# Kernel optimization log

Measured on AMD Instinct MI355X. Metric: run time of the kernel, lower is better.

Reference implementation:

```python
import jax, jax.numpy as jnp
import numpy as np

VOCAB, DIM, LAYERS, HEADS, FF, SEQ, BATCH = 32000, 1024, 4, 16, 4096, 2048, 2
HD = DIM // HEADS
EPS = 1e-6
ROPE_BASE = 10000.0


def setup_inputs() -> dict:
    key = jax.random.key(0)
    ks = jax.random.split(key, 10)
    std = 0.02
    return {
        "input_ids": jax.random.randint(ks[0], (BATCH, SEQ), 0, VOCAB, dtype=jnp.int32),
        "emb": jax.random.normal(ks[1], (VOCAB, DIM), jnp.float32) * std,
        "qkv_w": jax.random.normal(ks[2], (LAYERS, 3 * DIM, DIM), jnp.float32) * std,
        "out_w": jax.random.normal(ks[3], (LAYERS, DIM, DIM), jnp.float32) * std,
        "fc1_w": jax.random.normal(ks[4], (LAYERS, FF, DIM), jnp.float32) * std,
        "fc2_w": jax.random.normal(ks[5], (LAYERS, DIM, FF), jnp.float32) * std,
        "norm1_s": jnp.ones((LAYERS, DIM), jnp.float32),
        "norm2_s": jnp.ones((LAYERS, DIM), jnp.float32),
        "normf_s": jnp.ones((DIM,), jnp.float32),
        "lm_w": jax.random.normal(ks[6], (VOCAB, DIM), jnp.float32) * std,
    }


def _rms(x, scale):
    return x * jax.lax.rsqrt(jnp.mean(x * x, axis=-1, keepdims=True) + EPS) * scale


def _rope_tables(seq_len):
    inv_freq = 1.0 / (ROPE_BASE ** (jnp.arange(0, HD, 2, dtype=jnp.float32) / HD))
    freqs = jnp.arange(seq_len, dtype=jnp.float32)[:, None] * inv_freq[None, :]  # [S, HD/2]
    emb = jnp.concatenate([freqs, freqs], axis=-1)  # [S, HD]
    return jnp.cos(emb), jnp.sin(emb)


def _rotate_half(x):
    x1, x2 = jnp.split(x, 2, axis=-1)
    return jnp.concatenate([-x2, x1], axis=-1)


def _attention(h, qkv_w, out_w, cos, sin, mask):
    B, S, _ = h.shape
    qkv = jnp.einsum('bsd,ed->bse', h, qkv_w)  # [B, S, 3*DIM]
    qkv = qkv.reshape(B, S, 3, HEADS, HD).transpose(2, 0, 3, 1, 4)  # [3, B, H, S, hd]
    q, k, v = qkv[0], qkv[1], qkv[2]
    q = q * cos + _rotate_half(q) * sin
    k = k * cos + _rotate_half(k) * sin
    scores = jnp.einsum('bhqd,bhkd->bhqk', q, k) * (HD ** -0.5)
    scores = jnp.where(mask, scores, -jnp.inf)
    attn = jax.nn.softmax(scores, axis=-1)
    out = jnp.einsum('bhqk,bhkd->bhqd', attn, v)
    out = out.transpose(0, 2, 1, 3).reshape(B, S, DIM)
    return jnp.einsum('bsd,ed->bse', out, out_w)


def reference(input_ids, emb, qkv_w, out_w, fc1_w, fc2_w, norm1_s, norm2_s, normf_s, lm_w):
    B, S = input_ids.shape
    x = emb[input_ids]  # [B, S, DIM]
    cos, sin = _rope_tables(S)
    mask = jnp.tril(jnp.ones((S, S), dtype=bool))  # causal
    for l in range(LAYERS):
        x = x + _attention(_rms(x, norm1_s[l]), qkv_w[l], out_w[l], cos, sin, mask)
        h = _rms(x, norm2_s[l])
        ff = jnp.einsum('bsf,df->bsd', jax.nn.silu(jnp.einsum('bsd,fd->bsf', h, fc1_w[l])), fc2_w[l])
        x = x + ff
    logits = jnp.einsum('bsd,vd->bsv', _rms(x, normf_s), lm_w)
    return logits
```

## Files before the change

kernel.cpp:

```cpp
#include <hip/hip_runtime.h>

using u16 = unsigned short;
using u32 = unsigned int;
using bf16x8 = __attribute__((ext_vector_type(8))) __bf16;
using u16x8  = __attribute__((ext_vector_type(8))) u16;
using f32x4  = __attribute__((ext_vector_type(4))) float;
using u32x4  = __attribute__((ext_vector_type(4))) u32;

#define SEQ    2048
#define BATCH  2
#define DIM    1024
#define HEADS  16
#define HD     64
#define FF     4096
#define LAYERS 4
#define VOCAB  32000
#define ROWS   (BATCH*SEQ)

__device__ __forceinline__ u16 f2bf(float f) {
  u32 u = __float_as_uint(f);
  u += 0x7fffu + ((u >> 16) & 1u);
  return (u16)(u >> 16);
}
__device__ __forceinline__ float bf2f(u16 h) { return __uint_as_float(((u32)h) << 16); }

__device__ __forceinline__ void gload_lds16(const u16* g, u16* l) {
  __builtin_amdgcn_global_load_lds(
      (__attribute__((address_space(1))) void*)(u16*)g,
      (__attribute__((address_space(3))) void*)l, 16, 0, 0);
}

constexpr int BM = 128, BN = 128, BK = 32;

template<int EPI>
__global__ __launch_bounds__(256)
void gemm_nt(const u16* __restrict__ A, const u16* __restrict__ Bw,
             float* __restrict__ Cf, u16* __restrict__ Cb,
             int M, int N, int K, int KH)
{
  __shared__ __align__(16) u16 As[2][BM*BK];
  __shared__ __align__(16) u16 Bs[2][BN*BK];
  const int tid  = threadIdx.x;
  const int wid  = tid >> 6;
  const int lane = tid & 63;
  const int bn = blockIdx.x, bm = blockIdx.y;
  const int wm = wid >> 1, wn = wid & 1;

  if constexpr (EPI == 5) {
    const int z = blockIdx.z;
    A  += (size_t)z * KH;
    Bw += (size_t)z * KH;
    Cf += (size_t)z * M * N;
  }

  f32x4 acc[4][4] = {};

  const int lr = lane >> 2;
  const int lk = (lane & 3) * 8;
  const u16* Ag0 = A  + (size_t)(bm*BM + wid*16     + lr)*K + lk;
  const u16* Ag1 = A  + (size_t)(bm*BM + (wid+4)*16 + lr)*K + lk;
  const u16* Bg0 = Bw + (size_t)(bn*BN + wid*16     + lr)*K + lk;
  const u16* Bg1 = Bw + (size_t)(bn*BN + (wid+4)*16 + lr)*K + lk;

  auto STG = [&](int buf, int k0) {
    gload_lds16(Ag0 + k0, &As[buf][ wid   *512]);
    gload_lds16(Ag1 + k0, &As[buf][(wid+4)*512]);
    gload_lds16(Bg0 + k0, &Bs[buf][ wid   *512]);
    gload_lds16(Bg1 + k0, &Bs[buf][(wid+4)*512]);
  };

  const int aoff = (wm*64 + (lane & 15))*BK + (lane >> 4)*8;
  const int boff = (wn*64 + (lane & 15))*BK + (lane >> 4)*8;

  STG(0, 0);
  const int nt = KH / BK;
  for (int t = 0; t < nt; ++t) {
    __syncthreads();
    if (t + 1 < nt) STG((t+1) & 1, (t+1)*BK);
    const u16* Asf = &As[t & 1][aoff];
    const u16* Bsf = &Bs[t & 1][boff];
    bf16x8 af[4], bfr[4];
    #pragma unroll
    for (int m = 0; m < 4; ++m) af[m] = *(const bf16x8*)(Asf + m*16*BK);
    #pragma unroll
    for (int n = 0; n < 4; ++n) bfr[n] = *(const bf16x8*)(Bsf + n*16*BK);
    #pragma unroll
    for (int m = 0; m < 4; ++m)
      #pragma unroll
      for (int n = 0; n < 4; ++n)
        acc[m][n] = __builtin_amdgcn_mfma_f32_16x16x32_bf16(af[m], bfr[n], acc[m][n], 0, 0, 0);
  }

  const int row0 = bm*BM + wm*64 + (lane >> 4)*4;
  const int col0 = bn*BN + wn*64 + (lane & 15);
  #pragma unroll
  for (int m = 0; m < 4; ++m) {
    #pragma unroll
    for (int n = 0; n < 4; ++n) {
      #pragma unroll
      for (int r = 0; r < 4; ++r) {
        const size_t idx = (size_t)(row0 + m*16 + r)*N + (col0 + n*16);
        const float v = acc[m][n][r];
        if constexpr (EPI == 0)      Cf[idx] = v;
        else if constexpr (EPI == 1) Cf[idx] += v;
        else if constexpr (EPI == 2) Cb[idx] = f2bf(v / (1.f + __expf(-v)));
        else if constexpr (EPI == 5) Cf[idx] = v;
        else                         Cb[idx] = f2bf(v);
      }
    }
  }
}

__global__ __launch_bounds__(256)
void residual_add2(float* __restrict__ x, const float* __restrict__ p0,
                   const float* __restrict__ p1)
{
  const int i = blockIdx.x*256 + threadIdx.x;
  const float4 a = ((const float4*)x)[i];
  const float4 b = ((const float4*)p0)[i];
  const float4 c = ((const float4*)p1)[i];
  float4 o;
  o.x = a.x + b.x + c.x;
  o.y = a.y + b.y + c.y;
  o.z = a.z + b.z + c.z;
  o.w = a.w + b.w + c.w;
  ((float4*)x)[i] = o;
}

#define GPHASE(buf, q, STAGE_STMT, WAITV)                                     \
  {                                                                           \
    if ((q) == 0) {                                                           \
      _Pragma("unroll") for (int n = 0; n < 4; ++n)                           \
        _Pragma("unroll") for (int ks = 0; ks < 2; ++ks)                      \
          bfrag[n][ks] = ldsB((buf), wn*64 + n*16, ks);                       \
    }                                                                         \
    bf16x8 afrag[2][2];                                                       \
    _Pragma("unroll") for (int mi = 0; mi < 2; ++mi)                          \
      _Pragma("unroll") for (int ks = 0; ks < 2; ++ks)                        \
        afrag[mi][ks] = ldsA((buf), wm*128 + (q)*32 + mi*16, ks);             \
    STAGE_STMT;                                                               \
    __builtin_amdgcn_s_barrier();                                             \
    asm volatile("" ::: "memory");                                            \
    __builtin_amdgcn_s_setprio(1);                                            \
    _Pragma("unroll") for (int mi = 0; mi < 2; ++mi)                          \
      _Pragma("unroll") for (int n = 0; n < 4; ++n)                           \
        _Pragma("unroll") for (int ks = 0; ks < 2; ++ks)                      \
          acc[(q)*2+mi][n] = __builtin_amdgcn_mfma_f32_16x16x32_bf16(         \
              afrag[mi][ks], bfrag[n][ks], acc[(q)*2+mi][n], 0, 0, 0);        \
    __builtin_amdgcn_s_setprio(0);                                            \
    if ((WAITV) == 1) asm volatile("s_waitcnt vmcnt(6)" ::: "memory");        \
    if ((WAITV) == 2) asm volatile("s_waitcnt vmcnt(0)" ::: "memory");        \
    __builtin_amdgcn_s_barrier();                                             \
    asm volatile("" ::: "memory");                                            \
  }

template<int EPI>
__global__ __launch_bounds__(512, 2)
void gemm_nt_256(const u16* __restrict__ A, const u16* __restrict__ Bw,
                 float* __restrict__ Cf, u16* __restrict__ Cb,
                 u16* __restrict__ qbo, u16* __restrict__ kbo,
                 u16* __restrict__ vto, const float* __restrict__ tab,
                 int M, int N, int K, int nbm)
{
  __shared__ __align__(16) u16 lds[2][2][256*64];
  const int tid = threadIdx.x, wid = tid >> 6, lane = tid & 63;
  const int nwg = gridDim.x;
  const int swz = (blockIdx.x & 7)*(nwg >> 3) + (blockIdx.x >> 3);
  const int bm = swz % nbm, bn = swz / nbm;
  const int wm = wid >> 2, wn = wid & 3;

  f32x4 acc[8][4] = {};

  const int lrow = lane >> 3;
  const int lkel = ((lane & 7) ^ lrow) * 8;
  const u16* Abase = A  + (size_t)(bm*256)*K + lkel;
  const u16* Bbase = Bw + (size_t)(bn*256)*K + lkel;
  auto stageA = [&](int buf, int ha, int t) {
    const int r0 = ha*64 + 8*wid, r1 = 128 + ha*64 + 8*wid;
    const size_t ko = (size_t)t*64;
    gload_lds16(Abase + (size_t)(r0 + lrow)*K + ko, &lds[buf][0][r0*64]);
    gload_lds16(Abase + (size_t)(r1 + lrow)*K + ko, &lds[buf][0][r1*64]);
  };
  auto stageB = [&](int buf, int hb, int t) {
    const int r0 = hb*128 + 8*wid, r1 = hb*128 + 64 + 8*wid;
    const size_t ko = (size_t)t*64;
    gload_lds16(Bbase + (size_t)(r0 + lrow)*K + ko, &lds[buf][1][r0*64]);
    gload_lds16(Bbase + (size_t)(r1 + lrow)*K + ko, &lds[buf][1][r1*64]);
  };

  const int frow = lane & 15, g = lane >> 4;
  auto ldsA = [&](int buf, int rowbase, int ks) -> bf16x8 {
    return *(const bf16x8*)&lds[buf][0][(rowbase + frow)*64 + ((ks*4 + g) ^ (lane & 7))*8];
  };
  auto ldsB = [&](int buf, int rowbase, int ks) -> bf16x8 {
    return *(const bf16x8*)&lds[buf][1][(rowbase + frow)*64 + ((ks*4 + g) ^ (lane & 7))*8];
  };

  bf16x8 bfrag[4][2];
  const int NT = K / 64;

  stageB(0,0,0); stageB(0,1,0); stageA(0,0,0); stageA(0,1,0);
  stageB(1,0,1); stageB(1,1,1); stageA(1,0,1);
  asm volatile("s_waitcnt vmcnt(6)" ::: "memory");
  __builtin_amdgcn_s_barrier();
  asm volatile("" ::: "memory");

  for (int i = 0; i < NT/2 - 1; ++i) {
    const int t0 = 2*i;
    GPHASE(0, 0, stageA(1,1,t0+1), 0)
    GPHASE(0, 1, stageB(0,0,t0+2), 0)
    GPHASE(0, 2, stageB(0,1,t0+2), 0)
    GPHASE(0, 3, stageA(0,0,t0+2), 1)
    GPHASE(1, 0, stageA(0,1,t0+2), 0)
    GPHASE(1, 1, stageB(1,0,t0+3), 0)
    GPHASE(1, 2, stageB(1,1,t0+3), 0)
    GPHASE(1, 3, stageA(1,0,t0+3), 1)
  }
  GPHASE(0, 0, stageA(1,1,NT-1), 0)
  GPHASE(0, 1, ((void)0), 0)
  GPHASE(0, 2, ((void)0), 0)
  GPHASE(0, 3, ((void)0), 2)
  GPHASE(1, 0, ((void)0), 0)
  GPHASE(1, 1, ((void)0), 0)
  GPHASE(1, 2, ((void)0), 0)
  GPHASE(1, 3, ((void)0), 0)

  if constexpr (EPI == 4) {
    const int hc = bn*4 + wn;
    const int which = hc >> 4, h = hc & 15;
    const int brow0 = bm*256 + wm*128 + g*4;
    const int b = brow0 >> 11;
    const int bh = b*HEADS + h;
    if (which == 2) {
      #pragma unroll
      for (int mrep = 0; mrep < 8; ++mrep) {
        const int s = (brow0 + mrep*16) & (SEQ-1);
        #pragma unroll
        for (int n = 0; n < 4; ++n) {
          const int d = frow + n*16;
          ushort4 pk;
          pk.x = f2bf(acc[mrep][n][0]); pk.y = f2bf(acc[mrep][n][1]);
          pk.z = f2bf(acc[mrep][n][2]); pk.w = f2bf(acc[mrep][n][3]);
          *(ushort4*)&vto[((size_t)bh*64 + d)*SEQ + s] = pk;
        }
      }
    } else {
      u16* outb = (which == 0) ? qbo : kbo;
      const float qs = (which == 0) ? 0.125f : 1.f;
      #pragma unroll
      for (int mrep = 0; mrep < 8; ++mrep) {
        #pragma unroll
        for (int rr = 0; rr < 4; ++rr) {
          const int s = (brow0 + mrep*16 + rr) & (SEQ-1);
          const float c0 = tab[s*64 + frow],      s0v = tab[s*64 + 32 + frow];
          const float c1 = tab[s*64 + 16 + frow], s1v = tab[s*64 + 48 + frow];
          const float x0 = acc[mrep][0][rr], x1 = acc[mrep][1][rr];
          const float x2 = acc[mrep][2][rr], x3 = acc[mrep][3][rr];
          u16* orow = outb + ((size_t)bh*SEQ + s)*64;
          orow[frow]      = f2bf((x0*c0 - x2*s0v)*qs);
          orow[frow + 32] = f2bf((x2*c0 + x0*s0v)*qs);
          orow[frow + 16] = f2bf((x1*c1 - x3*s1v)*qs);
          orow[frow + 48] = f2bf((x3*c1 + x1*s1v)*qs);
        }
      }
    }
  } else {
    const int row0 = bm*256 + wm*128 + g*4;
    const int col0 = bn*256 + wn*64 + frow;
    #pragma unroll
    for (int mrep = 0; mrep < 8; ++mrep) {
      #pragma unroll
      for (int n = 0; n < 4; ++n) {
        #pragma unroll
        for (int r = 0; r < 4; ++r) {
          const size_t idx = (size_t)(row0 + mrep*16 + r)*N + (col0 + n*16);
          const float v = acc[mrep][n][r];
          if constexpr (EPI == 0)      Cf[idx] = v;
          else if constexpr (EPI == 2) Cb[idx] = f2bf(v / (1.f + __expf(-v)));
        }
      }
    }
  }
}

__global__ void cvt_f32_bf16(const float* __restrict__ in, u16* __restrict__ out, int n4)
{
  const int i = blockIdx.x*256 + threadIdx.x;
  if (i >= n4) return;
  const float4 v = ((const float4*)in)[i];
  ushort4 o;
  o.x = f2bf(v.x); o.y = f2bf(v.y); o.z = f2bf(v.z); o.w = f2bf(v.w);
  ((ushort4*)out)[i] = o;
}

__global__ void cvt_layer(const float* __restrict__ qw, const float* __restrict__ ow,
                          const float* __restrict__ f1, const float* __restrict__ f2,
                          u16* __restrict__ wq, u16* __restrict__ wo,
                          u16* __restrict__ w1, u16* __restrict__ w2)
{
  int i = blockIdx.x*256 + threadIdx.x;
  const float* src; u16* dst;
  if (i < 786432)       { src = qw; dst = wq; }
  else if (i < 1048576) { src = ow; dst = wo; i -= 786432; }
  else if (i < 2097152) { src = f1; dst = w1; i -= 1048576; }
  else                  { src = f2; dst = w2; i -= 2097152; }
  const float4 v = ((const float4*)src)[i];
  ushort4 o;
  o.x = f2bf(v.x); o.y = f2bf(v.y); o.z = f2bf(v.z); o.w = f2bf(v.w);
  ((ushort4*)dst)[i] = o;
}

__global__ void embed_gather(const int* __restrict__ ids, const float* __restrict__ emb,
                             float* __restrict__ x)
{
  const int row = blockIdx.x, t = threadIdx.x;
  const int id = ids[row];
  ((float4*)(x + (size_t)row*DIM))[t] = ((const float4*)(emb + (size_t)id*DIM))[t];
}

__global__ __launch_bounds__(256)
void rmsnorm_bf16(const float* __restrict__ x, const float* __restrict__ scale,
                  u16* __restrict__ out)
{
  const int row = blockIdx.x, t = threadIdx.x;
  const float4 v = ((const float4*)(x + (size_t)row*DIM))[t];
  float ss = v.x*v.x + v.y*v.y + v.z*v.z + v.w*v.w;
  #pragma unroll
  for (int off = 32; off; off >>= 1) ss += __shfl_xor(ss, off);
  __shared__ float red[4];
  if ((t & 63) == 0) red[t >> 6] = ss;
  __syncthreads();
  const float tot = red[0] + red[1] + red[2] + red[3];
  const float r = rsqrtf(tot * (1.f/(float)DIM) + 1e-6f);
  const float4 sc = ((const float4*)scale)[t];
  ushort4 o;
  o.x = f2bf(v.x * r * sc.x);
  o.y = f2bf(v.y * r * sc.y);
  o.z = f2bf(v.z * r * sc.z);
  o.w = f2bf(v.w * r * sc.w);
  ((ushort4*)(out + (size_t)row*DIM))[t] = o;
}

__global__ void rope_table(float* __restrict__ tab)
{
  const int idx = blockIdx.x*256 + threadIdx.x;
  const int s = idx >> 5, i = idx & 31;
  const float invf = powf(10000.f, -(float)i/32.f);
  const float f = (float)s * invf;
  tab[s*64 + i]      = cosf(f);
  tab[s*64 + 32 + i] = sinf(f);
}

__global__ __launch_bounds__(256, 4)
void attn_fwd(const u16* __restrict__ qb, const u16* __restrict__ kb,
              const u16* __restrict__ vt, u16* __restrict__ ctx)
{
  const int wid = threadIdx.x >> 6, lane = threadIdx.x & 63;
  const int bh = blockIdx.x >> 5, j = blockIdx.x & 31;
  const int qt = (wid == 0) ? j : (wid == 1) ? 63 - j : (wid == 2) ? 64 + j : 127 - j;
  const int q0 = qt * 16;
  const int g = lane >> 4, c15 = lane & 15;

  const u16* qbase = qb + (size_t)bh*SEQ*64;
  const u16* kbase = kb + (size_t)bh*SEQ*64;
  const u16* vtb   = vt + (size_t)bh*64*SEQ;

  const bf16x8 bQ0 = *(const bf16x8*)(qbase + (size_t)(q0 + c15)*64 + g*8);
  const bf16x8 bQ1 = *(const bf16x8*)(qbase + (size_t)(q0 + c15)*64 + 32 + g*8);

  f32x4 o[4] = {};
  float m = -INFINITY, lsum = 0.f;
  const int q_abs = q0 + c15;
  const int nt32 = (q0 >> 5) + 1;

  auto mk_aP = [&](const float* p) -> bf16x8 {
    const u32 pk00 = (u32)f2bf(p[0]) | ((u32)f2bf(p[1]) << 16);
    const u32 pk01 = (u32)f2bf(p[2]) | ((u32)f2bf(p[3]) << 16);
    const u32 pk10 = (u32)f2bf(p[4]) | ((u32)f2bf(p[5]) << 16);
    const u32 pk11 = (u32)f2bf(p[6]) | ((u32)f2bf(p[7]) << 16);
    u32 w[4];
    #pragma unroll
    for (int wi = 0; wi < 4; ++wi) {
      const int src = c15 | ((((g << 1) + (wi >> 1)) & 3) << 4);
      const u32 a0 = __shfl((wi & 1) ? pk01 : pk00, src);
      const u32 a1 = __shfl((wi & 1) ? pk11 : pk10, src);
      w[wi] = (g < 2) ? a0 : a1;
    }
    return __builtin_bit_cast(bf16x8, (u32x4){w[0], w[1], w[2], w[3]});
  };

  for (int t = 0; t < nt32; t += 2) {
    const int k0 = t*32;
    const bool haveB = (t + 1 < nt32);
    const bool diagA = (t     == nt32 - 1);
    const bool diagB = (t + 1 == nt32 - 1);

    const u16* kr0 = kbase + (size_t)(k0 + c15)*64 + g*8;
    const u16* kr1 = kbase + (size_t)(k0 + 16 + c15)*64 + g*8;
    const bf16x8 aK00 = *(const bf16x8*)(kr0);
    const bf16x8 aK01 = *(const bf16x8*)(kr0 + 32);
    const bf16x8 aK10 = *(const bf16x8*)(kr1);
    const bf16x8 aK11 = *(const bf16x8*)(kr1 + 32);
    bf16x8 aK20{}, aK21{}, aK30{}, aK31{};
    if (haveB) {
      const u16* kr2 = kbase + (size_t)(k0 + 32 + c15)*64 + g*8;
      const u16* kr3 = kbase + (size_t)(k0 + 48 + c15)*64 + g*8;
      aK20 = *(const bf16x8*)(kr2);
      aK21 = *(const bf16x8*)(kr2 + 32);
      aK30 = *(const bf16x8*)(kr3);
      aK31 = *(const bf16x8*)(kr3 + 32);
    }
    bf16x8 vvA[4];
    #pragma unroll
    for (int dh = 0; dh < 4; ++dh)
      vvA[dh] = *(const bf16x8*)(vtb + (size_t)(dh*16 + c15)*SEQ + k0 + g*8);

    const f32x4 z = {};
    f32x4 sc0 = __builtin_amdgcn_mfma_f32_16x16x32_bf16(aK00, bQ0, z, 0,0,0);
    sc0 = __builtin_amdgcn_mfma_f32_16x16x32_bf16(aK01, bQ1, sc0, 0,0,0);
    f32x4 sc1 = __builtin_amdgcn_mfma_f32_16x16x32_bf16(aK10, bQ0, z, 0,0,0);
    sc1 = __builtin_amdgcn_mfma_f32_16x16x32_bf16(aK11, bQ1, sc1, 0,0,0);
    f32x4 sc2 = z, sc3 = z;
    if (haveB) {
      sc2 = __builtin_amdgcn_mfma_f32_16x16x32_bf16(aK20, bQ0, z, 0,0,0);
      sc2 = __builtin_amdgcn_mfma_f32_16x16x32_bf16(aK21, bQ1, sc2, 0,0,0);
      sc3 = __builtin_amdgcn_mfma_f32_16x16x32_bf16(aK30, bQ0, z, 0,0,0);
      sc3 = __builtin_amdgcn_mfma_f32_16x16x32_bf16(aK31, bQ1, sc3, 0,0,0);
    }
    bf16x8 vvB[4] = {};
    if (haveB) {
      #pragma unroll
      for (int dh = 0; dh < 4; ++dh)
        vvB[dh] = *(const bf16x8*)(vtb + (size_t)(dh*16 + c15)*SEQ + k0 + 32 + g*8);
    }

    float s[16];
    if (diagA) {
      #pragma unroll
      for (int r = 0; r < 4; ++r) {
        s[r]   = (k0 + 4*g + r      > q_abs) ? -INFINITY : sc0[r];
        s[4+r] = (k0 + 16 + 4*g + r > q_abs) ? -INFINITY : sc1[r];
      }
    } else {
      #pragma unroll
      for (int r = 0; r < 4; ++r) { s[r] = sc0[r]; s[4+r] = sc1[r]; }
    }
    if (!haveB) {
      #pragma unroll
      for (int r = 0; r < 8; ++r) s[8+r] = -INFINITY;
    } else if (diagB) {
      #pragma unroll
      for (int r = 0; r < 4; ++r) {
        s[8+r]  = (k0 + 32 + 4*g + r > q_abs) ? -INFINITY : sc2[r];
        s[12+r] = (k0 + 48 + 4*g + r > q_abs) ? -INFINITY : sc3[r];
      }
    } else {
      #pragma unroll
      for (int r = 0; r < 4; ++r) { s[8+r] = sc2[r]; s[12+r] = sc3[r]; }
    }

    float tm = s[0];
    #pragma unroll
    for (int r = 1; r < 16; ++r) tm = fmaxf(tm, s[r]);
    tm = fmaxf(tm, __shfl_xor(tm, 16));
    tm = fmaxf(tm, __shfl_xor(tm, 32));

    if (!__all(tm <= m + 8.f)) {
      const float mnew = fmaxf(m, tm);
      const float corr = __expf(m - mnew);
      lsum *= corr;
      float corrq[4];
      #pragma unroll
      for (int r = 0; r < 4; ++r) corrq[r] = __shfl(corr, 4*g + r);
      #pragma unroll
      for (int dh = 0; dh < 4; ++dh)
        #pragma unroll
        for (int r = 0; r < 4; ++r) o[dh][r] *= corrq[r];
      m = mnew;
    }

    float p[16];
    #pragma unroll
    for (int r = 0; r < 16; ++r) p[r] = __expf(s[r] - m);
    float ps = 0.f;
    #pragma unroll
    for (int r = 0; r < 16; ++r) ps += p[r];
    ps += __shfl_xor(ps, 16);
    ps += __shfl_xor(ps, 32);
    lsum += ps;

    const bf16x8 aPA = mk_aP(&p[0]);
    #pragma unroll
    for (int dh = 0; dh < 4; ++dh)
      o[dh] = __builtin_amdgcn_mfma_f32_16x16x32_bf16(aPA, vvA[dh], o[dh], 0,0,0);
    if (haveB) {
      const bf16x8 aPB = mk_aP(&p[8]);
      #pragma unroll
      for (int dh = 0; dh < 4; ++dh)
        o[dh] = __builtin_amdgcn_mfma_f32_16x16x32_bf16(aPB, vvB[dh], o[dh], 0,0,0);
    }
  }

  float linv[4];
  #pragma unroll
  for (int r = 0; r < 4; ++r) linv[r] = 1.f / __shfl(lsum, 4*g + r);
  const int b = bh >> 4, h = bh & 15;
  #pragma unroll
  for (int r = 0; r < 4; ++r) {
    u16* crow = ctx + ((size_t)(b*SEQ + q0 + 4*g + r))*DIM + h*HD + c15;
    #pragma unroll
    for (int dh = 0; dh < 4; ++dh) crow[dh*16] = f2bf(o[dh][r] * linv[r]);
  }
}

extern "C" void kernel_launch(void* const* d_in, const int* in_sizes, int n_in,
                              void* d_out, int out_size, void* d_ws, size_t ws_size,
                              hipStream_t stream)
{
  const int*   ids   = (const int*)  d_in[0];
  const float* emb   = (const float*)d_in[1];
  const float* qkv_w = (const float*)d_in[2];
  const float* out_w = (const float*)d_in[3];
  const float* fc1_w = (const float*)d_in[4];
  const float* fc2_w = (const float*)d_in[5];
  const float* n1    = (const float*)d_in[6];
  const float* n2    = (const float*)d_in[7];
  const float* nf    = (const float*)d_in[8];
  const float* lm_w  = (const float*)d_in[9];
  float* logits = (float*)d_out;

  char* ws = (char*)d_ws;
  size_t off = 0;
  auto walloc = [&](size_t bytes) -> void* {
    void* p = ws + off;
    off += (bytes + 255) & ~(size_t)255;
    return p;
  };
  float* x     = (float*)walloc((size_t)ROWS*DIM*4);
  u16*   hbf   = (u16*)  walloc((size_t)ROWS*DIM*2);
  u16*   ctxbf = (u16*)  walloc((size_t)ROWS*DIM*2);
  u16*   gbf   = (u16*)  walloc((size_t)ROWS*FF*2);
  u16*   wq    = (u16*)  walloc((size_t)3*DIM*DIM*2);
  u16*   wo    = (u16*)  walloc((size_t)DIM*DIM*2);
  u16*   w1    = (u16*)  walloc((size_t)FF*DIM*2);
  u16*   w2    = (u16*)  walloc((size_t)DIM*FF*2);
  float* tab   = (float*)walloc((size_t)SEQ*64*4);
  float* fpart = (float*)walloc((size_t)2*ROWS*DIM*4);
  u16* qbuf = (u16*)gbf;
  u16* kbuf = qbuf + (size_t)ROWS*DIM;
  u16* vtbuf= kbuf + (size_t)ROWS*DIM;
  u16* wlm = (u16*)ctxbf;

  rope_table<<<SEQ*32/256, 256, 0, stream>>>(tab);
  embed_gather<<<ROWS, 256, 0, stream>>>(ids, emb, x);

  for (int l = 0; l < LAYERS; ++l) {
    cvt_layer<<<3145728/256, 256, 0, stream>>>(
        qkv_w + (size_t)l*3*DIM*DIM, out_w + (size_t)l*DIM*DIM,
        fc1_w + (size_t)l*FF*DIM,    fc2_w + (size_t)l*DIM*FF,
        wq, wo, w1, w2);

    rmsnorm_bf16<<<ROWS, 256, 0, stream>>>(x, n1 + l*DIM, hbf);
    gemm_nt_256<4><<<(3*DIM/256)*(ROWS/256), 512, 0, stream>>>(
        hbf, wq, nullptr, nullptr, qbuf, kbuf, vtbuf, tab, ROWS, 3*DIM, DIM, ROWS/256);
    attn_fwd<<<BATCH*HEADS*(SEQ/64), 256, 0, stream>>>(qbuf, kbuf, vtbuf, ctxbf);
    gemm_nt<1><<<dim3(DIM/BN, ROWS/BM), 256, 0, stream>>>(ctxbf, wo, x, nullptr, ROWS, DIM, DIM, DIM);

    rmsnorm_bf16<<<ROWS, 256, 0, stream>>>(x, n2 + l*DIM, hbf);
    gemm_nt_256<2><<<(FF/256)*(ROWS/256), 512, 0, stream>>>(
        hbf, w1, nullptr, gbf, nullptr, nullptr, nullptr, nullptr, ROWS, FF, DIM, ROWS/256);
    gemm_nt<5><<<dim3(DIM/BN, ROWS/BM, 2), 256, 0, stream>>>(gbf, w2, fpart, nullptr, ROWS, DIM, FF, FF/2);
    residual_add2<<<ROWS*DIM/4/256, 256, 0, stream>>>(x, fpart, fpart + (size_t)ROWS*DIM);
  }

  rmsnorm_bf16<<<ROWS, 256, 0, stream>>>(x, nf, hbf);
  cvt_f32_bf16<<<VOCAB*DIM/4/256, 256, 0, stream>>>(lm_w, wlm, VOCAB*DIM/4);
  gemm_nt_256<0><<<(VOCAB/256)*(ROWS/256), 512, 0, stream>>>(
      hbf, wlm, logits, nullptr, nullptr, nullptr, nullptr, nullptr, ROWS, VOCAB, DIM, ROWS/256);
}
```

Baseline: 1.656 ms.

## Fuse residual add with RMSNorm and split-K the attention output projection

New measurement: 1.599 ms (median of 2 runs). -3.5%, faster.

```diff
diff --git a/kernel.cpp b/kernel.cpp
--- a/kernel.cpp
+++ b/kernel.cpp
@@ -112,19 +112,35 @@
 }
 
 __global__ __launch_bounds__(256)
-void residual_add2(float* __restrict__ x, const float* __restrict__ p0,
-                   const float* __restrict__ p1)
-{
-  const int i = blockIdx.x*256 + threadIdx.x;
-  const float4 a = ((const float4*)x)[i];
+void residual_add2_norm(float* __restrict__ x, const float* __restrict__ p0,
+                        const float* __restrict__ p1,
+                        const float* __restrict__ scale, u16* __restrict__ out)
+{
+  const int row = blockIdx.x, t = threadIdx.x;
+  const size_t i = (size_t)row*(DIM/4) + t;
+  float4 a = ((const float4*)x)[i];
   const float4 b = ((const float4*)p0)[i];
   const float4 c = ((const float4*)p1)[i];
-  float4 o;
-  o.x = a.x + b.x + c.x;
-  o.y = a.y + b.y + c.y;
-  o.z = a.z + b.z + c.z;
-  o.w = a.w + b.w + c.w;
-  ((float4*)x)[i] = o;
+  a.x += b.x + c.x;
+  a.y += b.y + c.y;
+  a.z += b.z + c.z;
+  a.w += b.w + c.w;
+  ((float4*)x)[i] = a;
+  float ss = a.x*a.x + a.y*a.y + a.z*a.z + a.w*a.w;
+  #pragma unroll
+  for (int off = 32; off; off >>= 1) ss += __shfl_xor(ss, off);
+  __shared__ float red[4];
+  if ((t & 63) == 0) red[t >> 6] = ss;
+  __syncthreads();
+  const float tot = red[0] + red[1] + red[2] + red[3];
+  const float r = rsqrtf(tot * (1.f/(float)DIM) + 1e-6f);
+  const float4 sc = ((const float4*)scale)[t];
+  ushort4 o;
+  o.x = f2bf(a.x * r * sc.x);
+  o.y = f2bf(a.y * r * sc.y);
+  o.z = f2bf(a.z * r * sc.z);
+  o.w = f2bf(a.w * r * sc.w);
+  ((ushort4*)(out + (size_t)row*DIM))[t] = o;
 }
 
 #define GPHASE(buf, q, STAGE_STMT, WAITV)                                     \
@@ -553,6 +569,7 @@
 
   rope_table<<<SEQ*32/256, 256, 0, stream>>>(tab);
   embed_gather<<<ROWS, 256, 0, stream>>>(ids, emb, x);
+  rmsnorm_bf16<<<ROWS, 256, 0, stream>>>(x, n1, hbf);
 
   for (int l = 0; l < LAYERS; ++l) {
     cvt_layer<<<3145728/256, 256, 0, stream>>>(
@@ -560,20 +577,21 @@
         fc1_w + (size_t)l*FF*DIM,    fc2_w + (size_t)l*DIM*FF,
         wq, wo, w1, w2);
 
-    rmsnorm_bf16<<<ROWS, 256, 0, stream>>>(x, n1 + l*DIM, hbf);
     gemm_nt_256<4><<<(3*DIM/256)*(ROWS/256), 512, 0, stream>>>(
         hbf, wq, nullptr, nullptr, qbuf, kbuf, vtbuf, tab, ROWS, 3*DIM, DIM, ROWS/256);
     attn_fwd<<<BATCH*HEADS*(SEQ/64), 256, 0, stream>>>(qbuf, kbuf, vtbuf, ctxbf);
-    gemm_nt<1><<<dim3(DIM/BN, ROWS/BM), 256, 0, stream>>>(ctxbf, wo, x, nullptr, ROWS, DIM, DIM, DIM);
-
-    rmsnorm_bf16<<<ROWS, 256, 0, stream>>>(x, n2 + l*DIM, hbf);
+    gemm_nt<5><<<dim3(DIM/BN, ROWS/BM, 2), 256, 0, stream>>>(ctxbf, wo, fpart, nullptr, ROWS, DIM, DIM, DIM/2);
+    residual_add2_norm<<<ROWS, 256, 0, stream>>>(x, fpart, fpart + (size_t)ROWS*DIM,
+                                                 n2 + l*DIM, hbf);
+
     gemm_nt_256<2><<<(FF/256)*(ROWS/256), 512, 0, stream>>>(
         hbf, w1, nullptr, gbf, nullptr, nullptr, nullptr, nullptr, ROWS, FF, DIM, ROWS/256);
     gemm_nt<5><<<dim3(DIM/BN, ROWS/BM, 2), 256, 0, stream>>>(gbf, w2, fpart, nullptr, ROWS, DIM, FF, FF/2);
-    residual_add2<<<ROWS*DIM/4/256, 256, 0, stream>>>(x, fpart, fpart + (size_t)ROWS*DIM);
-  }
-
-  rmsnorm_bf16<<<ROWS, 256, 0, stream>>>(x, nf, hbf);
+    const float* nxt = (l < LAYERS-1) ? (n1 + (size_t)(l+1)*DIM) : nf;
+    residual_add2_norm<<<ROWS, 256, 0, stream>>>(x, fpart, fpart + (size_t)ROWS*DIM,
+                                                 nxt, hbf);
+  }
+
   cvt_f32_bf16<<<VOCAB*DIM/4/256, 256, 0, stream>>>(lm_w, wlm, VOCAB*DIM/4);
   gemm_nt_256<0><<<(VOCAB/256)*(ROWS/256), 512, 0, stream>>>(
       hbf, wlm, logits, nullptr, nullptr, nullptr, nullptr, nullptr, ROWS, VOCAB, DIM, ROWS/256);
```
